# Kernel tuning notes

Hardware: AMD Instinct MI355X
Metric: run time of the kernel (lower is better)

Reference implementation:

```python
import jax, jax.numpy as jnp
import numpy as np

SEQ, DM, STATE, BATCH = 1024, 512, 16, 8
D2 = 2 * DM
EPS = 1e-5


def rmsnorm(x, w):
    return x * jax.lax.rsqrt(jnp.mean(x * x, axis=-1, keepdims=True) + EPS) * w


def setup_inputs() -> dict:
    key = jax.random.key(0)
    ks = jax.random.split(key, 16)
    def lin(k, i, o):
        k1, k2 = jax.random.split(k)
        s = 1.0 / np.sqrt(i)
        return (jax.random.uniform(k1, (i, o), minval=-s, maxval=s),
                jax.random.uniform(k2, (o,), minval=-s, maxval=s))
    inp_w, inp_b = lin(ks[0], DM, D2)
    convlin_w, convlin_b = lin(ks[1], D2, D2)
    fc1_w, fc1_b = lin(ks[2], D2, D2)
    fc2_w, fc2_b = lin(ks[3], D2, STATE)
    fc3_w, fc3_b = lin(ks[4], D2, STATE)
    D_w, D_b = lin(ks[5], DM, D2)
    out_w, _ = lin(ks[6], D2, DM)
    out_b = jnp.ones((DM,))  # nn.init.constant_(out_proj.bias, 1.0)
    # Conv1d(seq_len, seq_len, k=3): weight (out_ch=SEQ, in_ch=SEQ, 3)
    s = 1.0 / np.sqrt(SEQ * 3)
    conv_w = jax.random.uniform(ks[7], (SEQ, SEQ, 3), minval=-s, maxval=s)
    conv_b = jax.random.uniform(ks[8], (SEQ,), minval=-s, maxval=s)
    norm_w = jnp.ones((DM,))
    x = jax.random.normal(ks[9], (BATCH, SEQ, DM))
    return dict(x=x, norm_w=norm_w, inp_w=inp_w, inp_b=inp_b, conv_w=conv_w,
                conv_b=conv_b, convlin_w=convlin_w, convlin_b=convlin_b,
                fc1_w=fc1_w, fc1_b=fc1_b, fc2_w=fc2_w, fc2_b=fc2_b,
                fc3_w=fc3_w, fc3_b=fc3_b, D_w=D_w, D_b=D_b,
                out_w=out_w, out_b=out_b)


def reference(x, norm_w, inp_w, inp_b, conv_w, conv_b, convlin_w, convlin_b,
              fc1_w, fc1_b, fc2_w, fc2_b, fc3_w, fc3_b, D_w, D_b, out_w, out_b):
    xn = rmsnorm(x, norm_w)                                  # (b, L, d)
    x_proj = xn @ inp_w + inp_b                              # (b, L, 2d)
    # Conv1d over channels=seq_len, spatial=2d, padding=1
    x_conv = jax.lax.conv_general_dilated(
        x_proj, conv_w, window_strides=(1,), padding=[(1, 1)],
        dimension_numbers=('NCH', 'OIH', 'NCH')) + conv_b[None, :, None]
    x_conv_out = jax.nn.silu(x_conv) @ convlin_w + convlin_b  # (b, L, 2d)
    # S6: h starts at zero so dA term vanishes; y = x*delta*sum_n(B*C)
    u = x_conv_out
    B = u @ fc2_w + fc2_b                                     # (b, L, n)
    C = u @ fc3_w + fc3_b                                     # (b, L, n)
    delta = jax.nn.softplus(u @ fc1_w + fc1_b)                # (b, L, 2d)
    bc = jnp.sum(B * C, axis=-1, keepdims=True)               # (b, L, 1)
    x_ssm = u * delta * bc                                    # (b, L, 2d)
    x_act = jax.nn.silu(x_ssm)
    x_residual = jax.nn.silu(xn @ D_w + D_b)
    return (x_residual * x_act) @ out_w + out_b               # (b, L, d)
```

## Files before the change

kernel.cpp:

```cpp
#include <hip/hip_runtime.h>
#include <hip/hip_bf16.h>

#define SEQ 1024
#define DM 512
#define D2 1024
#define NSTATE 16
#define BATCH 8
#define ROWS (BATCH * SEQ)
#define EPSF 1e-5f

typedef __attribute__((ext_vector_type(8))) short bf16x8;
typedef __attribute__((ext_vector_type(4))) float f32x4;

#define AS1 __attribute__((address_space(1)))
#define AS3 __attribute__((address_space(3)))

__device__ __forceinline__ void gll16(const void* g, void* l) {
    __builtin_amdgcn_global_load_lds(
        (const AS1 unsigned int*)(uintptr_t)g,
        (AS3 unsigned int*)(unsigned int)(uintptr_t)l, 16, 0, 0);
}

__device__ __forceinline__ float sigmoidf_(float x) {
    return 1.f / (1.f + __expf(-x));
}
__device__ __forceinline__ unsigned short f2bf(float f) {
    __hip_bfloat16 h = __float2bfloat16(f);
    unsigned short r;
    __builtin_memcpy(&r, &h, 2);
    return r;
}

__global__ __launch_bounds__(256) void prep_all(
    const float* s0, const float* s1, const float* s2, const float* s3,
    const float* s4, const float* s5, const float* s6,
    __hip_bfloat16* d0, __hip_bfloat16* d1, __hip_bfloat16* d2,
    __hip_bfloat16* d3, __hip_bfloat16* d4, __hip_bfloat16* d5,
    __hip_bfloat16* d6) {
    const int j = blockIdx.z;
    int R, C;
    const float* src;
    __hip_bfloat16* dst;
    switch (j) {
        case 0: src = s0; dst = d0; R = 512; C = 1024; break;
        case 1: src = s1; dst = d1; R = 512; C = 1024; break;
        case 2: src = s2; dst = d2; R = 1024; C = 1024; break;
        case 3: src = s3; dst = d3; R = 1024; C = 1024; break;
        case 4: src = s4; dst = d4; R = 1024; C = 512; break;
        case 5: src = s5; dst = d5; R = 1024; C = 16; break;
        default: src = s6; dst = d6; R = 1024; C = 16; break;
    }
    int c0 = blockIdx.x * 32, r0 = blockIdx.y * 32;
    if (c0 >= C || r0 >= R) return;
    __shared__ float tile[32][33];
    int tx = threadIdx.x & 31, ty = threadIdx.x >> 5;
#pragma unroll
    for (int p = 0; p < 4; ++p) {
        int r = r0 + ty + p * 8, c = c0 + tx;
        if (r < R && c < C) tile[ty + p * 8][tx] = src[(size_t)r * C + c];
    }
    __syncthreads();
#pragma unroll
    for (int p = 0; p < 4; ++p) {
        int c = c0 + ty + p * 8, r = r0 + tx;
        if (r < R && c < C)
            dst[(size_t)c * R + r] = __float2bfloat16(tile[tx][ty + p * 8]);
    }
}

__global__ __launch_bounds__(256) void convw_k(const float* __restrict__ cw,
                                               __hip_bfloat16* __restrict__ wk) {
    int idx = blockIdx.x * 256 + threadIdx.x;
    float a = cw[(size_t)idx * 3 + 0];
    float b = cw[(size_t)idx * 3 + 1];
    float c = cw[(size_t)idx * 3 + 2];
    wk[idx] = __float2bfloat16(a);
    wk[(size_t)SEQ * SEQ + idx] = __float2bfloat16(b);
    wk[(size_t)2 * SEQ * SEQ + idx] = __float2bfloat16(c);
}

__global__ __launch_bounds__(256) void rmsnorm_k(
    const float* __restrict__ x, const float* __restrict__ w,
    __hip_bfloat16* __restrict__ o) {
    int row = blockIdx.x;
    const float* xr = x + (size_t)row * DM;
    __hip_bfloat16* orow = o + (size_t)row * DM;
    int t = threadIdx.x;
    float v0 = xr[t];
    float v1 = xr[t + 256];
    float ss = v0 * v0 + v1 * v1;
#pragma unroll
    for (int off = 32; off; off >>= 1) ss += __shfl_down(ss, off, 64);
    __shared__ float parts[4];
    if ((t & 63) == 0) parts[t >> 6] = ss;
    __syncthreads();
    float tot = parts[0] + parts[1] + parts[2] + parts[3];
    float rs = rsqrtf(tot * (1.f / DM) + EPSF);
    orow[t] = __float2bfloat16(v0 * rs * w[t]);
    orow[t + 256] = __float2bfloat16(v1 * rs * w[t + 256]);
}

template <int EPI>
__global__ __launch_bounds__(256) void mgemm(
    const __hip_bfloat16* __restrict__ A, const __hip_bfloat16* __restrict__ Bt,
    const float* __restrict__ bias, void* __restrict__ outp,
    void* __restrict__ outp2, const float* __restrict__ bias2,
    const __hip_bfloat16* __restrict__ uptr,
    const __hip_bfloat16* __restrict__ resid, const float* __restrict__ bcv,
    int M, int N, int K) {
    __shared__ __align__(16) __hip_bfloat16 As[3][128 * 32];
    __shared__ __align__(16) __hip_bfloat16 Bs[3][128 * 32];
    const int nbx = gridDim.x;
    int lin = blockIdx.y * nbx + blockIdx.x;
    int chunk = (nbx * gridDim.y) >> 3;
    int wg = (lin & 7) * chunk + (lin >> 3);
    const int n0 = (wg % nbx) * 128, m0 = (wg / nbx) * 128;
    const int t = threadIdx.x, lane = t & 63, w = t >> 6;
    const int wr = w >> 1, wc = w & 1;
    const int l15 = lane & 15, l4 = lane >> 4;

    const int r0_ = t >> 2, c0_ = (t & 3) ^ ((r0_ >> 1) & 3);
    const int b1 = 256 + t, r1_ = b1 >> 2, c1_ = (b1 & 3) ^ ((r1_ >> 1) & 3);
    const __hip_bfloat16* gA0 = A + (size_t)(m0 + r0_) * K + c0_ * 8;
    const __hip_bfloat16* gA1 = A + (size_t)(m0 + r1_) * K + c1_ * 8;
    const __hip_bfloat16* gB0 = Bt + (size_t)(n0 + r0_) * K + c0_ * 8;
    const __hip_bfloat16* gB1 = Bt + (size_t)(n0 + r1_) * K + c1_ * 8;
    const int d0 = (w * 64) * 8, d1 = (256 + w * 64) * 8;

    int offA[4], offB[4];
#pragma unroll
    for (int i = 0; i < 4; ++i) {
        int ra = wr * 64 + i * 16 + l15;
        offA[i] = (ra * 4 + (l4 ^ ((ra >> 1) & 3))) * 8;
        int rb = wc * 64 + i * 16 + l15;
        offB[i] = (rb * 4 + (l4 ^ ((rb >> 1) & 3))) * 8;
    }

#define MSTAGE(BUF, K0)                  \
    {                                    \
        gll16(gA0 + (K0), &As[BUF][d0]); \
        gll16(gA1 + (K0), &As[BUF][d1]); \
        gll16(gB0 + (K0), &Bs[BUF][d0]); \
        gll16(gB1 + (K0), &Bs[BUF][d1]); \
    }

    f32x4 acc[4][4] = {};
    const int NT = K >> 5;
    unsigned curb = 0, nxtb = 1, thdb = 2;
    MSTAGE(0, 0);
    MSTAGE(1, 32);
    asm volatile("s_waitcnt vmcnt(4)" ::: "memory");
    __builtin_amdgcn_s_barrier();
    __builtin_amdgcn_sched_barrier(0);

#pragma unroll 1
    for (int kt = 0; kt < NT; ++kt) {
        const bool st = (kt + 2 < NT);
        if (st) MSTAGE(thdb, (kt + 2) * 32);
        bf16x8 af[4], bv[4];
#pragma unroll
        for (int i = 0; i < 4; ++i) {
            af[i] = *(const bf16x8*)&As[curb][offA[i]];
            bv[i] = *(const bf16x8*)&Bs[curb][offB[i]];
        }
        __builtin_amdgcn_s_setprio(1);
#pragma unroll
        for (int i = 0; i < 4; ++i)
#pragma unroll
            for (int j = 0; j < 4; ++j)
                acc[i][j] = __builtin_amdgcn_mfma_f32_16x16x32_bf16(
                    af[i], bv[j], acc[i][j], 0, 0, 0);
        __builtin_amdgcn_s_setprio(0);
        if (kt + 1 < NT) {
            if (st)
                asm volatile("s_waitcnt vmcnt(4)" ::: "memory");
            else
                asm volatile("s_waitcnt vmcnt(0)" ::: "memory");
            __builtin_amdgcn_s_barrier();
            __builtin_amdgcn_sched_barrier(0);
        }
        unsigned tb = curb;
        curb = nxtb;
        nxtb = thdb;
        thdb = tb;
    }
#undef MSTAGE

    const int mb = m0 + wr * 64, nb = n0 + wc * 64;
#pragma unroll
    for (int i = 0; i < 4; ++i) {
#pragma unroll
        for (int j = 0; j < 4; ++j) {
            int ngl = nb + j * 16 + l15;
            if (EPI == 5) {
                if (nb < D2) {
                    float bj = bias[ngl];
                    int b = m0 >> 10;
                    int ibase = (mb & (SEQ - 1)) + i * 16 + l4 * 4;
                    ushort4 pk;
                    pk.x = f2bf(acc[i][j][0] + bj);
                    pk.y = f2bf(acc[i][j][1] + bj);
                    pk.z = f2bf(acc[i][j][2] + bj);
                    pk.w = f2bf(acc[i][j][3] + bj);
                    *(ushort4*)((__hip_bfloat16*)outp +
                                ((size_t)b * D2 + ngl) * SEQ + ibase) = pk;
                } else {
                    int ng2 = ngl - D2;
                    float bj = bias2[ng2];
#pragma unroll
                    for (int r = 0; r < 4; ++r) {
                        int mg = mb + i * 16 + l4 * 4 + r;
                        float c = acc[i][j][r] + bj;
                        ((__hip_bfloat16*)outp2)[(size_t)mg * D2 + ng2] =
                            __float2bfloat16(c * sigmoidf_(c));
                    }
                }
            } else {
                float bj = bias[ngl];
#pragma unroll
                for (int r = 0; r < 4; ++r) {
                    int mg = mb + i * 16 + l4 * 4 + r;
                    size_t ro = (size_t)mg * N + ngl;
                    float c = acc[i][j][r] + bj;
                    if (EPI == 1) {
                        ((__hip_bfloat16*)outp)[ro] = __float2bfloat16(c);
                    } else if (EPI == 3) {
                        float sp = (c > 20.f) ? c : log1pf(__expf(c));
                        float xs = __bfloat162float(uptr[ro]) * sp * bcv[mg];
                        float v = __bfloat162float(resid[ro]) *
                                  (xs * sigmoidf_(xs));
                        ((__hip_bfloat16*)outp)[ro] = __float2bfloat16(v);
                    } else {
                        ((float*)outp)[ro] = c;
                    }
                }
            }
        }
    }
}

__global__ __launch_bounds__(256) void conv_mfma(
    const __hip_bfloat16* __restrict__ wk,
    const __hip_bfloat16* __restrict__ Xt,
    const float* __restrict__ cb, __hip_bfloat16* __restrict__ outp) {
    __shared__ __align__(16) __hip_bfloat16 Ws[2][3][128 * 32];
    __shared__ __align__(16) __hip_bfloat16 Xs[2][128 * 32];
    __shared__ __align__(16) __hip_bfloat16 Xh[2][SEQ];
    int lin = blockIdx.x + 8 * blockIdx.y + 64 * blockIdx.z;
    int wg = (lin & 7) * 64 + (lin >> 3);
    const int n0 = (wg & 7) * 128;
    const int m0 = ((wg >> 3) & 7) * 128;
    const int z = wg >> 6;
    const int t = threadIdx.x, lane = t & 63, w = t >> 6;
    const int wr = w >> 1, wc = w & 1;
    const int l15 = lane & 15, l4 = lane >> 4;
    const __hip_bfloat16* Xtb = Xt + (size_t)z * D2 * SEQ;

    {
        int which = t >> 7;
        int col = (t & 127) * 8;
        int h = n0 - 1 + which * 129;
        uint4 v = make_uint4(0u, 0u, 0u, 0u);
        if (h >= 0 && h < D2)
            v = *(const uint4*)(Xtb + (size_t)h * SEQ + col);
        *(uint4*)&Xh[which][col] = v;
    }

    int rowp[2], cbw[2];
#pragma unroll
    for (int p = 0; p < 2; ++p) {
        int blk = p * 256 + t;
        rowp[p] = blk >> 2;
        cbw[p] = (blk & 3) ^ ((rowp[p] >> 1) & 3);
    }
    const __hip_bfloat16* wsrc[2][3];
    const __hip_bfloat16* xsrc[2];
#pragma unroll
    for (int p = 0; p < 2; ++p) {
#pragma unroll
        for (int tp = 0; tp < 3; ++tp)
            wsrc[p][tp] = wk + (size_t)tp * SEQ * SEQ +
                          (size_t)(m0 + rowp[p]) * SEQ + cbw[p] * 8;
        xsrc[p] = Xtb + (size_t)(n0 + rowp[p]) * SEQ + cbw[p] * 8;
    }
    const int dst0 = (w * 64) * 8, dst1 = (256 + w * 64) * 8;

    int offA[4];
#pragma unroll
    for (int i = 0; i < 4; ++i) {
        int ra = wr * 64 + i * 16 + l15;
        offA[i] = (ra * 4 + (l4 ^ ((ra >> 1) & 3))) * 8;
    }

#define CSTAGE(BUF, K0)                              \
    {                                                \
        gll16(wsrc[0][0] + (K0), &Ws[BUF][0][dst0]); \
        gll16(wsrc[1][0] + (K0), &Ws[BUF][0][dst1]); \
        gll16(wsrc[0][1] + (K0), &Ws[BUF][1][dst0]); \
        gll16(wsrc[1][1] + (K0), &Ws[BUF][1][dst1]); \
        gll16(wsrc[0][2] + (K0), &Ws[BUF][2][dst0]); \
        gll16(wsrc[1][2] + (K0), &Ws[BUF][2][dst1]); \
        gll16(xsrc[0] + (K0), &Xs[BUF][dst0]);       \
        gll16(xsrc[1] + (K0), &Xs[BUF][dst1]);       \
    }

    f32x4 acc[4][4] = {};
    CSTAGE(0, 0);
    asm volatile("s_waitcnt lgkmcnt(0)" ::: "memory");

#pragma unroll 1
    for (int kt = 0; kt < 32; ++kt) {
        const int k0 = kt * 32;
        const int buf = kt & 1;
        if (kt + 1 < 32) {
            CSTAGE(buf ^ 1, (kt + 1) * 32);
            asm volatile("s_waitcnt vmcnt(8)" ::: "memory");
        } else {
            asm volatile("s_waitcnt vmcnt(0)" ::: "memory");
        }
        __builtin_amdgcn_s_barrier();
        __builtin_amdgcn_sched_barrier(0);
        bf16x8 aw[3][4];
#pragma unroll
        for (int tp = 0; tp < 3; ++tp)
#pragma unroll
            for (int i = 0; i < 4; ++i)
                aw[tp][i] = *(const bf16x8*)&Ws[buf][tp][offA[i]];
        __builtin_amdgcn_s_setprio(1);
#pragma unroll
        for (int j = 0; j < 4; ++j) {
#pragma unroll
            for (int tp = 0; tp < 3; ++tp) {
                int rb = wc * 64 + j * 16 + l15 + tp;
                int r = rb - 1;
                const __hip_bfloat16* src =
                    &Xs[buf][(r * 4 + (l4 ^ ((r >> 1) & 3))) * 8];
                if (rb == 0) src = &Xh[0][k0 + l4 * 8];
                if (rb == 129) src = &Xh[1][k0 + l4 * 8];
                bf16x8 bvx = *(const bf16x8*)src;
#pragma unroll
                for (int i = 0; i < 4; ++i)
                    acc[i][j] = __builtin_amdgcn_mfma_f32_16x16x32_bf16(
                        aw[tp][i], bvx, acc[i][j], 0, 0, 0);
            }
        }
        __builtin_amdgcn_s_setprio(0);
        if (kt + 1 < 32) {
            __builtin_amdgcn_s_barrier();
            __builtin_amdgcn_sched_barrier(0);
        }
    }
#undef CSTAGE

    const int mb = m0 + wr * 64, nb = n0 + wc * 64;
    size_t ob = (size_t)z * SEQ * D2;
#pragma unroll
    for (int i = 0; i < 4; ++i)
#pragma unroll
        for (int j = 0; j < 4; ++j)
#pragma unroll
            for (int r = 0; r < 4; ++r) {
                int mg = mb + i * 16 + l4 * 4 + r;
                int ng = nb + j * 16 + l15;
                float c = acc[i][j][r] + cb[mg];
                outp[ob + (size_t)mg * D2 + ng] =
                    __float2bfloat16(c * sigmoidf_(c));
            }
}

__global__ __launch_bounds__(256) void bc2_k(
    const __hip_bfloat16* __restrict__ u, const __hip_bfloat16* __restrict__ fcT,
    const float* __restrict__ b2, const float* __restrict__ b3,
    float* __restrict__ bc) {
    __shared__ __align__(16) __hip_bfloat16 Bl[32 * 1024];
    __shared__ __align__(16) __hip_bfloat16 As[3][128 * 32];
    const int m0 = blockIdx.x * 128;
    const int t = threadIdx.x, lane = t & 63, w = t >> 6;
    const int l15 = lane & 15, l4 = lane >> 4;

#pragma unroll
    for (int it = 0; it < 16; ++it) {
        int q = it * 256 + t;
        int n = q >> 7, blk = q & 127;
        uint4 v = *(const uint4*)(fcT + (size_t)n * 1024 + blk * 8);
        *(uint4*)&Bl[(n * 128 + (blk ^ (n & 7))) * 8] = v;
    }

    const int r0_ = t >> 2, c0_ = (t & 3) ^ ((r0_ >> 1) & 3);
    const int bq = 256 + t, r1_ = bq >> 2, c1_ = (bq & 3) ^ ((r1_ >> 1) & 3);
    const __hip_bfloat16* gA0 = u + (size_t)(m0 + r0_) * 1024 + c0_ * 8;
    const __hip_bfloat16* gA1 = u + (size_t)(m0 + r1_) * 1024 + c1_ * 8;
    const int d0 = (w * 64) * 8, d1 = (256 + w * 64) * 8;

    int offA[2];
#pragma unroll
    for (int i = 0; i < 2; ++i) {
        int ra = w * 32 + i * 16 + l15;
        offA[i] = (ra * 4 + (l4 ^ ((ra >> 1) & 3))) * 8;
    }

#define BSTAGE(BUF, K0)                  \
    {                                    \
        gll16(gA0 + (K0), &As[BUF][d0]); \
        gll16(gA1 + (K0), &As[BUF][d1]); \
    }

    f32x4 acc[2][2] = {};
    unsigned curb = 0, nxtb = 1, thdb = 2;
    BSTAGE(0, 0);
    BSTAGE(1, 32);
    asm volatile("s_waitcnt vmcnt(2)" ::: "memory");
    __builtin_amdgcn_s_barrier();
    __builtin_amdgcn_sched_barrier(0);

#pragma unroll 1
    for (int kt = 0; kt < 32; ++kt) {
        const bool st = (kt + 2 < 32);
        if (st) BSTAGE(thdb, (kt + 2) * 32);
        bf16x8 af[2], bf[2];
#pragma unroll
        for (int i = 0; i < 2; ++i) af[i] = *(const bf16x8*)&As[curb][offA[i]];
#pragma unroll
        for (int nj = 0; nj < 2; ++nj) {
            int n = nj * 16 + l15;
            int blk = (kt * 4 + l4) ^ (n & 7);
            bf[nj] = *(const bf16x8*)&Bl[(n * 128 + blk) * 8];
        }
#pragma unroll
        for (int i = 0; i < 2; ++i)
#pragma unroll
            for (int nj = 0; nj < 2; ++nj)
                acc[i][nj] = __builtin_amdgcn_mfma_f32_16x16x32_bf16(
                    af[i], bf[nj], acc[i][nj], 0, 0, 0);
        if (kt + 1 < 32) {
            if (st)
                asm volatile("s_waitcnt vmcnt(2)" ::: "memory");
            else
                asm volatile("s_waitcnt vmcnt(0)" ::: "memory");
            __builtin_amdgcn_s_barrier();
            __builtin_amdgcn_sched_barrier(0);
        }
        unsigned tb = curb;
        curb = nxtb;
        nxtb = thdb;
        thdb = tb;
    }
#undef BSTAGE

    float bb2 = b2[l15], bb3 = b3[l15];
#pragma unroll
    for (int i = 0; i < 2; ++i)
#pragma unroll
        for (int r = 0; r < 4; ++r) {
            float Bv = acc[i][0][r] + bb2;
            float Cv = acc[i][1][r] + bb3;
            float p = Bv * Cv;
            p += __shfl_xor(p, 1, 64);
            p += __shfl_xor(p, 2, 64);
            p += __shfl_xor(p, 4, 64);
            p += __shfl_xor(p, 8, 64);
            if (l15 == 0)
                bc[m0 + w * 32 + i * 16 + l4 * 4 + r] = p;
        }
}

extern "C" void kernel_launch(void* const* d_in, const int* in_sizes, int n_in,
                              void* d_out, int out_size, void* d_ws,
                              size_t ws_size, hipStream_t stream) {
    const float* x = (const float*)d_in[0];
    const float* norm_w = (const float*)d_in[1];
    const float* inp_w = (const float*)d_in[2];
    const float* inp_b = (const float*)d_in[3];
    const float* conv_w = (const float*)d_in[4];
    const float* conv_b = (const float*)d_in[5];
    const float* convlin_w = (const float*)d_in[6];
    const float* convlin_b = (const float*)d_in[7];
    const float* fc1_w = (const float*)d_in[8];
    const float* fc1_b = (const float*)d_in[9];
    const float* fc2_w = (const float*)d_in[10];
    const float* fc2_b = (const float*)d_in[11];
    const float* fc3_w = (const float*)d_in[12];
    const float* fc3_b = (const float*)d_in[13];
    const float* D_w = (const float*)d_in[14];
    const float* D_b = (const float*)d_in[15];
    const float* out_w = (const float*)d_in[16];
    const float* out_b = (const float*)d_in[17];
    float* out = (float*)d_out;

    __hip_bfloat16* xnb = (__hip_bfloat16*)d_ws;
    __hip_bfloat16* xt = xnb + (size_t)ROWS * DM;
    __hip_bfloat16* cvo = xt + (size_t)BATCH * D2 * SEQ;
    __hip_bfloat16* u = cvo + (size_t)ROWS * D2;
    __hip_bfloat16* resid = u + (size_t)ROWS * D2;
    __hip_bfloat16* Wcat = resid + (size_t)ROWS * D2;
    __hip_bfloat16* clT = Wcat + (size_t)2 * D2 * DM;
    __hip_bfloat16* fc1T = clT + (size_t)D2 * D2;
    __hip_bfloat16* outT = fc1T + (size_t)D2 * D2;
    __hip_bfloat16* wk = outT + (size_t)DM * D2;
    __hip_bfloat16* fcT = wk + (size_t)3 * SEQ * SEQ;
    float* bcb = (float*)(fcT + (size_t)32 * D2);

    prep_all<<<dim3(32, 32, 7), 256, 0, stream>>>(
        inp_w, D_w, convlin_w, fc1_w, out_w, fc2_w, fc3_w, Wcat,
        Wcat + (size_t)D2 * DM, clT, fc1T, outT, fcT, fcT + (size_t)16 * D2);
    convw_k<<<SEQ * SEQ / 256, 256, 0, stream>>>(conv_w, wk);
    rmsnorm_k<<<ROWS, 256, 0, stream>>>(x, norm_w, xnb);
    mgemm<5><<<dim3(2 * D2 / 128, ROWS / 128), 256, 0, stream>>>(
        xnb, Wcat, inp_b, xt, resid, D_b, nullptr, nullptr, nullptr, ROWS,
        2 * D2, DM);
    conv_mfma<<<dim3(D2 / 128, SEQ / 128, BATCH), 256, 0, stream>>>(
        wk, xt, conv_b, cvo);
    mgemm<1><<<dim3(D2 / 128, ROWS / 128), 256, 0, stream>>>(
        cvo, clT, convlin_b, u, nullptr, nullptr, nullptr, nullptr, nullptr,
        ROWS, D2, D2);
    bc2_k<<<ROWS / 128, 256, 0, stream>>>(u, fcT, fc2_b, fc3_b, bcb);
    mgemm<3><<<dim3(D2 / 128, ROWS / 128), 256, 0, stream>>>(
        u, fc1T, fc1_b, cvo, nullptr, nullptr, u, resid, bcb, ROWS, D2, D2);
    mgemm<4><<<dim3(DM / 128, ROWS / 128), 256, 0, stream>>>(
        cvo, outT, out_b, out, nullptr, nullptr, nullptr, nullptr, nullptr,
        ROWS, DM, D2);
}
```

Before: 225.0 us.

## Enlarge GEMM K-tile to 128 with double-buffered LDS and new swizzle

Switches the bf16 MFMA GEMM from a 3-stage pipeline of 32-wide K tiles to a 2-stage pipeline of 128-wide K tiles. Each stage issues 16 direct global-to-LDS loads per thread and uses an 8-way XOR swizzle. This is meant to cut the number of barriers and loop iterations per K. In exchange, LDS use per block grows to 128KB, which limits residency to one block per CU, and the shallower pipeline exposes more load latency at the start of the loop.

After: 268.6 us. +19.4%, slower.

```diff
diff --git a/kernel.cpp b/kernel.cpp
--- a/kernel.cpp
+++ b/kernel.cpp
@@ -108,8 +108,8 @@
     const __hip_bfloat16* __restrict__ uptr,
     const __hip_bfloat16* __restrict__ resid, const float* __restrict__ bcv,
     int M, int N, int K) {
-    __shared__ __align__(16) __hip_bfloat16 As[3][128 * 32];
-    __shared__ __align__(16) __hip_bfloat16 Bs[3][128 * 32];
+    __shared__ __align__(16) __hip_bfloat16 As[2][128 * 128];
+    __shared__ __align__(16) __hip_bfloat16 Bs[2][128 * 128];
     const int nbx = gridDim.x;
     int lin = blockIdx.y * nbx + blockIdx.x;
     int chunk = (nbx * gridDim.y) >> 3;
@@ -119,70 +119,73 @@
     const int wr = w >> 1, wc = w & 1;
     const int l15 = lane & 15, l4 = lane >> 4;
 
-    const int r0_ = t >> 2, c0_ = (t & 3) ^ ((r0_ >> 1) & 3);
-    const int b1 = 256 + t, r1_ = b1 >> 2, c1_ = (b1 & 3) ^ ((r1_ >> 1) & 3);
-    const __hip_bfloat16* gA0 = A + (size_t)(m0 + r0_) * K + c0_ * 8;
-    const __hip_bfloat16* gA1 = A + (size_t)(m0 + r1_) * K + c1_ * 8;
-    const __hip_bfloat16* gB0 = Bt + (size_t)(n0 + r0_) * K + c0_ * 8;
-    const __hip_bfloat16* gB1 = Bt + (size_t)(n0 + r1_) * K + c1_ * 8;
-    const int d0 = (w * 64) * 8, d1 = (256 + w * 64) * 8;
-
-    int offA[4], offB[4];
+    const __hip_bfloat16* srcA[8];
+    const __hip_bfloat16* srcB[8];
+#pragma unroll
+    for (int p = 0; p < 8; ++p) {
+        int q = p * 256 + t, r = q >> 4;
+        int cs = (q & 8) | ((q & 7) ^ (r & 7));
+        srcA[p] = A + (size_t)(m0 + r) * K + cs * 8;
+        srcB[p] = Bt + (size_t)(n0 + r) * K + cs * 8;
+    }
+
+    int offA[4][4], offB[4][4];
 #pragma unroll
     for (int i = 0; i < 4; ++i) {
         int ra = wr * 64 + i * 16 + l15;
-        offA[i] = (ra * 4 + (l4 ^ ((ra >> 1) & 3))) * 8;
         int rb = wc * 64 + i * 16 + l15;
-        offB[i] = (rb * 4 + (l4 ^ ((rb >> 1) & 3))) * 8;
-    }
-
-#define MSTAGE(BUF, K0)                  \
-    {                                    \
-        gll16(gA0 + (K0), &As[BUF][d0]); \
-        gll16(gA1 + (K0), &As[BUF][d1]); \
-        gll16(gB0 + (K0), &Bs[BUF][d0]); \
-        gll16(gB1 + (K0), &Bs[BUF][d1]); \
+#pragma unroll
+        for (int kk = 0; kk < 4; ++kk) {
+            int b = kk * 4 + l4;
+            offA[i][kk] = (ra * 16 + (b & 8) + ((b & 7) ^ (ra & 7))) * 8;
+            offB[i][kk] = (rb * 16 + (b & 8) + ((b & 7) ^ (rb & 7))) * 8;
+        }
+    }
+
+#define MSTAGE(BUF, K0)                                           \
+    {                                                             \
+        _Pragma("unroll") for (int p = 0; p < 8; ++p) {           \
+            gll16(srcA[p] + (K0), &As[BUF][(p * 256 + w * 64) * 8]); \
+            gll16(srcB[p] + (K0), &Bs[BUF][(p * 256 + w * 64) * 8]); \
+        }                                                         \
     }
 
     f32x4 acc[4][4] = {};
-    const int NT = K >> 5;
-    unsigned curb = 0, nxtb = 1, thdb = 2;
+    const int NT = K >> 7;
     MSTAGE(0, 0);
-    MSTAGE(1, 32);
-    asm volatile("s_waitcnt vmcnt(4)" ::: "memory");
-    __builtin_amdgcn_s_barrier();
-    __builtin_amdgcn_sched_barrier(0);
 
 #pragma unroll 1
     for (int kt = 0; kt < NT; ++kt) {
-        const bool st = (kt + 2 < NT);
-        if (st) MSTAGE(thdb, (kt + 2) * 32);
-        bf16x8 af[4], bv[4];
-#pragma unroll
-        for (int i = 0; i < 4; ++i) {
-            af[i] = *(const bf16x8*)&As[curb][offA[i]];
-            bv[i] = *(const bf16x8*)&Bs[curb][offB[i]];
-        }
-        __builtin_amdgcn_s_setprio(1);
-#pragma unroll
-        for (int i = 0; i < 4; ++i)
-#pragma unroll
-            for (int j = 0; j < 4; ++j)
-                acc[i][j] = __builtin_amdgcn_mfma_f32_16x16x32_bf16(
-                    af[i], bv[j], acc[i][j], 0, 0, 0);
-        __builtin_amdgcn_s_setprio(0);
+        const int buf = kt & 1;
         if (kt + 1 < NT) {
-            if (st)
-                asm volatile("s_waitcnt vmcnt(4)" ::: "memory");
-            else
-                asm volatile("s_waitcnt vmcnt(0)" ::: "memory");
+            MSTAGE(buf ^ 1, (kt + 1) * 128);
+            asm volatile("s_waitcnt vmcnt(16)" ::: "memory");
+        } else {
+            asm volatile("s_waitcnt vmcnt(0)" ::: "memory");
+        }
+        __builtin_amdgcn_s_barrier();
+        __builtin_amdgcn_sched_barrier(0);
+#pragma unroll
+        for (int kk = 0; kk < 4; ++kk) {
+            bf16x8 af[4], bv[4];
+#pragma unroll
+            for (int i = 0; i < 4; ++i) {
+                af[i] = *(const bf16x8*)&As[buf][offA[i][kk]];
+                bv[i] = *(const bf16x8*)&Bs[buf][offB[i][kk]];
+            }
+            __builtin_amdgcn_s_setprio(1);
+#pragma unroll
+            for (int i = 0; i < 4; ++i)
+#pragma unroll
+                for (int j = 0; j < 4; ++j)
+                    acc[i][j] = __builtin_amdgcn_mfma_f32_16x16x32_bf16(
+                        af[i], bv[j], acc[i][j], 0, 0, 0);
+            __builtin_amdgcn_s_setprio(0);
+        }
+        if (kt + 1 < NT) {
             __builtin_amdgcn_s_barrier();
             __builtin_amdgcn_sched_barrier(0);
         }
-        unsigned tb = curb;
-        curb = nxtb;
-        nxtb = thdb;
-        thdb = tb;
     }
 #undef MSTAGE
 
```

## Process two K-slices per barrier in GEMM with 4-buffer LDS ring

Applied to the files above, without the earlier changes.

Restructures the mgemm main loop to consume two 32-wide K slices per iteration from a four-stage LDS ring, prefetching two slices ahead, and makes K a compile-time template parameter. The goal is to halve barrier and wait overhead and give the scheduler a larger MFMA block. In exchange it raises LDS usage per block and now waits for all outstanding loads, including the fresh prefetch, before each barrier, which can reduce load/compute overlap.

Result: no change. 224.4 us, median of 2 (-0.2%).

```diff
diff --git a/kernel.cpp b/kernel.cpp
--- a/kernel.cpp
+++ b/kernel.cpp
@@ -100,16 +100,16 @@
     orow[t + 256] = __float2bfloat16(v1 * rs * w[t + 256]);
 }
 
-template <int EPI>
+template <int EPI, int KC>
 __global__ __launch_bounds__(256) void mgemm(
     const __hip_bfloat16* __restrict__ A, const __hip_bfloat16* __restrict__ Bt,
     const float* __restrict__ bias, void* __restrict__ outp,
     void* __restrict__ outp2, const float* __restrict__ bias2,
     const __hip_bfloat16* __restrict__ uptr,
     const __hip_bfloat16* __restrict__ resid, const float* __restrict__ bcv,
-    int M, int N, int K) {
-    __shared__ __align__(16) __hip_bfloat16 As[3][128 * 32];
-    __shared__ __align__(16) __hip_bfloat16 Bs[3][128 * 32];
+    int M, int N) {
+    __shared__ __align__(16) __hip_bfloat16 As[4][128 * 32];
+    __shared__ __align__(16) __hip_bfloat16 Bs[4][128 * 32];
     const int nbx = gridDim.x;
     int lin = blockIdx.y * nbx + blockIdx.x;
     int chunk = (nbx * gridDim.y) >> 3;
@@ -121,10 +121,10 @@
 
     const int r0_ = t >> 2, c0_ = (t & 3) ^ ((r0_ >> 1) & 3);
     const int b1 = 256 + t, r1_ = b1 >> 2, c1_ = (b1 & 3) ^ ((r1_ >> 1) & 3);
-    const __hip_bfloat16* gA0 = A + (size_t)(m0 + r0_) * K + c0_ * 8;
-    const __hip_bfloat16* gA1 = A + (size_t)(m0 + r1_) * K + c1_ * 8;
-    const __hip_bfloat16* gB0 = Bt + (size_t)(n0 + r0_) * K + c0_ * 8;
-    const __hip_bfloat16* gB1 = Bt + (size_t)(n0 + r1_) * K + c1_ * 8;
+    const __hip_bfloat16* gA0 = A + (size_t)(m0 + r0_) * KC + c0_ * 8;
+    const __hip_bfloat16* gA1 = A + (size_t)(m0 + r1_) * KC + c1_ * 8;
+    const __hip_bfloat16* gB0 = Bt + (size_t)(n0 + r0_) * KC + c0_ * 8;
+    const __hip_bfloat16* gB1 = Bt + (size_t)(n0 + r1_) * KC + c1_ * 8;
     const int d0 = (w * 64) * 8, d1 = (256 + w * 64) * 8;
 
     int offA[4], offB[4];
@@ -145,23 +145,31 @@
     }
 
     f32x4 acc[4][4] = {};
-    const int NT = K >> 5;
-    unsigned curb = 0, nxtb = 1, thdb = 2;
+    constexpr int NT = KC >> 6;
     MSTAGE(0, 0);
     MSTAGE(1, 32);
-    asm volatile("s_waitcnt vmcnt(4)" ::: "memory");
+    asm volatile("s_waitcnt vmcnt(0)" ::: "memory");
     __builtin_amdgcn_s_barrier();
     __builtin_amdgcn_sched_barrier(0);
 
 #pragma unroll 1
-    for (int kt = 0; kt < NT; ++kt) {
-        const bool st = (kt + 2 < NT);
-        if (st) MSTAGE(thdb, (kt + 2) * 32);
-        bf16x8 af[4], bv[4];
+    for (int p = 0; p < NT; ++p) {
+        const int kA = 2 * p, kB = 2 * p + 1;
+        const int bufA = kA & 3, bufB = kB & 3;
+        if (p + 1 < NT) {
+            MSTAGE((kA + 2) & 3, (kA + 2) * 32);
+            MSTAGE((kB + 2) & 3, (kB + 2) * 32);
+        }
+        bf16x8 a0[4], b0[4], a1[4], b1v[4];
 #pragma unroll
         for (int i = 0; i < 4; ++i) {
-            af[i] = *(const bf16x8*)&As[curb][offA[i]];
-            bv[i] = *(const bf16x8*)&Bs[curb][offB[i]];
+            a0[i] = *(const bf16x8*)&As[bufA][offA[i]];
+            b0[i] = *(const bf16x8*)&Bs[bufA][offB[i]];
+        }
+#pragma unroll
+        for (int i = 0; i < 4; ++i) {
+            a1[i] = *(const bf16x8*)&As[bufB][offA[i]];
+            b1v[i] = *(const bf16x8*)&Bs[bufB][offB[i]];
         }
         __builtin_amdgcn_s_setprio(1);
 #pragma unroll
@@ -169,20 +177,19 @@
 #pragma unroll
             for (int j = 0; j < 4; ++j)
                 acc[i][j] = __builtin_amdgcn_mfma_f32_16x16x32_bf16(
-                    af[i], bv[j], acc[i][j], 0, 0, 0);
+                    a0[i], b0[j], acc[i][j], 0, 0, 0);
+#pragma unroll
+        for (int i = 0; i < 4; ++i)
+#pragma unroll
+            for (int j = 0; j < 4; ++j)
+                acc[i][j] = __builtin_amdgcn_mfma_f32_16x16x32_bf16(
+                    a1[i], b1v[j], acc[i][j], 0, 0, 0);
         __builtin_amdgcn_s_setprio(0);
-        if (kt + 1 < NT) {
-            if (st)
-                asm volatile("s_waitcnt vmcnt(4)" ::: "memory");
-            else
-                asm volatile("s_waitcnt vmcnt(0)" ::: "memory");
+        if (p + 1 < NT) {
+            asm volatile("s_waitcnt vmcnt(0)" ::: "memory");
             __builtin_amdgcn_s_barrier();
             __builtin_amdgcn_sched_barrier(0);
         }
-        unsigned tb = curb;
-        curb = nxtb;
-        nxtb = thdb;
-        thdb = tb;
     }
 #undef MSTAGE
 
@@ -505,18 +512,18 @@
         Wcat + (size_t)D2 * DM, clT, fc1T, outT, fcT, fcT + (size_t)16 * D2);
     convw_k<<<SEQ * SEQ / 256, 256, 0, stream>>>(conv_w, wk);
     rmsnorm_k<<<ROWS, 256, 0, stream>>>(x, norm_w, xnb);
-    mgemm<5><<<dim3(2 * D2 / 128, ROWS / 128), 256, 0, stream>>>(
+    mgemm<5, DM><<<dim3(2 * D2 / 128, ROWS / 128), 256, 0, stream>>>(
         xnb, Wcat, inp_b, xt, resid, D_b, nullptr, nullptr, nullptr, ROWS,
-        2 * D2, DM);
+        2 * D2);
     conv_mfma<<<dim3(D2 / 128, SEQ / 128, BATCH), 256, 0, stream>>>(
         wk, xt, conv_b, cvo);
-    mgemm<1><<<dim3(D2 / 128, ROWS / 128), 256, 0, stream>>>(
+    mgemm<1, D2><<<dim3(D2 / 128, ROWS / 128), 256, 0, stream>>>(
         cvo, clT, convlin_b, u, nullptr, nullptr, nullptr, nullptr, nullptr,
-        ROWS, D2, D2);
+        ROWS, D2);
     bc2_k<<<ROWS / 128, 256, 0, stream>>>(u, fcT, fc2_b, fc3_b, bcb);
-    mgemm<3><<<dim3(D2 / 128, ROWS / 128), 256, 0, stream>>>(
-        u, fc1T, fc1_b, cvo, nullptr, nullptr, u, resid, bcb, ROWS, D2, D2);
-    mgemm<4><<<dim3(DM / 128, ROWS / 128), 256, 0, stream>>>(
+    mgemm<3, D2><<<dim3(D2 / 128, ROWS / 128), 256, 0, stream>>>(
+        u, fc1T, fc1_b, cvo, nullptr, nullptr, u, resid, bcb, ROWS, D2);
+    mgemm<4, D2><<<dim3(DM / 128, ROWS / 128), 256, 0, stream>>>(
         cvo, outT, out_b, out, nullptr, nullptr, nullptr, nullptr, nullptr,
-        ROWS, DM, D2);
-}
+        ROWS, DM);
+}
```
